# Optimization experiments

Measured on AMD Instinct MI355X. Metric: run time of the kernel, lower is better.

## Reference

```python
import jax, jax.numpy as jnp
import numpy as np

N_EMBD = 768
HEAD_SIZE = 64
B, T = 8, 4096


def setup_inputs() -> dict:
    key = jax.random.key(0)
    ks = jax.random.split(key, 7)
    s = 0.02  # small init scale for weights
    return {
        "x": jax.random.normal(ks[0], (B, T, N_EMBD), dtype=jnp.float32),
        "Wq": jax.random.normal(ks[1], (N_EMBD, HEAD_SIZE), dtype=jnp.float32) * s,
        "bq": jax.random.normal(ks[2], (HEAD_SIZE,), dtype=jnp.float32) * s,
        "Wk": jax.random.normal(ks[3], (N_EMBD, HEAD_SIZE), dtype=jnp.float32) * s,
        "bk": jax.random.normal(ks[4], (HEAD_SIZE,), dtype=jnp.float32) * s,
        "Wv": jax.random.normal(ks[5], (N_EMBD, HEAD_SIZE), dtype=jnp.float32) * s,
        "bv": jax.random.normal(ks[6], (HEAD_SIZE,), dtype=jnp.float32) * s,
    }


def reference(x, Wq, bq, Wk, bk, Wv, bv):
    # x: [B, T, C]; note: scale uses C = n_embd (input dim), per the original code.
    C = x.shape[-1]
    scale = jnp.asarray(C, x.dtype) ** -0.5
    q = x @ Wq + bq  # [B, T, H]
    k = x @ Wk + bk  # [B, T, H]
    v = x @ Wv + bv  # [B, T, H]
    wei = jnp.einsum("bqh,bkh->bqk", q, k) * scale  # [B, T, T]
    att = jax.nn.softmax(wei, axis=-1)
    # dropout p=0.0 (eval mode) -> identity
    out = jnp.einsum("bqk,bkh->bqh", att, v)  # [B, T, H]
    return out
```

## Files before the change

### kernel.cpp

```cpp
#include <hip/hip_runtime.h>
#include <stdint.h>

#define T_SEQ 4096
#define CEMB 768
#define HS 64

typedef __attribute__((ext_vector_type(8))) short bf16x8;
typedef __attribute__((ext_vector_type(16))) float f32x16;
typedef __attribute__((ext_vector_type(4))) unsigned int u32x4;

__device__ __forceinline__ short bfru(float f) {
    uint32_t u = __builtin_bit_cast(uint32_t, f);
    return (short)((u + 0x8000u) >> 16);
}
__device__ __forceinline__ uint32_t cvtpk_bf16(float lo, float hi) {
    uint32_t r;
    asm("v_cvt_pk_bf16_f32 %0, %1, %2" : "=v"(r) : "v"(lo), "v"(hi));
    return r;
}

#define QSCALE (0.036084391824351615f * 1.4426950408889634f)

__global__ __launch_bounds__(256) void prep_wt(const float* __restrict__ Wq,
                                               const float* __restrict__ Wk,
                                               const float* __restrict__ Wv,
                                               short* __restrict__ wtf) {
    const int p = blockIdx.x;
    const int tid = threadIdx.x;
    const int lane = tid & 63, jp = tid >> 6;
    const int l31 = lane & 31, lhi = lane >> 5;
    const int kq = p % 48, ct = p / 48;
    const int k = kq * 16 + lhi * 8 + jp * 2;
    const int nn = ct * 32 + l31;
    const float* W = nn < 64 ? Wq : (nn < 128 ? Wk : Wv);
    const int col = nn & 63;
    uint32_t lo = (uint16_t)bfru(W[k * 64 + col]);
    uint32_t hi = (uint16_t)bfru(W[(k + 1) * 64 + col]);
    *(uint32_t*)&wtf[(p * 64 + lane) * 8 + jp * 2] = lo | (hi << 16);
}

__global__ __launch_bounds__(256) void qkv_proj(const float* __restrict__ x,
        const float* __restrict__ bq, const float* __restrict__ bk, const float* __restrict__ bv,
        const short* __restrict__ wtf,
        short* __restrict__ qo, short* __restrict__ ko, short* __restrict__ vto) {
    __shared__ short S[64 * 72];

    const int tid  = threadIdx.x;
    const int wave = tid >> 6, lane = tid & 63;
    const int l31  = lane & 31, lhi = lane >> 5;
    const int rg   = wave & 1;
    const int ctb  = (wave >> 1) * 3;
    const int rowbase = blockIdx.x * 64;

    f32x16 acc[3];
    #pragma unroll
    for (int c = 0; c < 3; ++c) {
        const int ct = ctb + c, nn = ct * 32 + l31;
        const float bb = nn < 64 ? bq[nn] : (nn < 128 ? bk[nn - 64] : bv[nn - 128]);
        #pragma unroll
        for (int r = 0; r < 16; ++r) acc[c][r] = bb;
    }

    const int sr = tid >> 2, sseg = (tid & 3) * 16;
    for (int kt = 0; kt < 12; ++kt) {
        const float4* src = (const float4*)(x + (long)(rowbase + sr) * CEMB + kt * 64 + sseg);
        float4 f0 = src[0], f1 = src[1], f2 = src[2], f3 = src[3];
        bf16x8 w0, w1;
        w0[0]=bfru(f0.x); w0[1]=bfru(f0.y); w0[2]=bfru(f0.z); w0[3]=bfru(f0.w);
        w0[4]=bfru(f1.x); w0[5]=bfru(f1.y); w0[6]=bfru(f1.z); w0[7]=bfru(f1.w);
        w1[0]=bfru(f2.x); w1[1]=bfru(f2.y); w1[2]=bfru(f2.z); w1[3]=bfru(f2.w);
        w1[4]=bfru(f3.x); w1[5]=bfru(f3.y); w1[6]=bfru(f3.z); w1[7]=bfru(f3.w);
        *(bf16x8*)&S[sr * 72 + sseg]     = w0;
        *(bf16x8*)&S[sr * 72 + sseg + 8] = w1;
        __syncthreads();
        #pragma unroll
        for (int kc = 0; kc < 4; ++kc) {
            bf16x8 af = *(const bf16x8*)&S[(rg * 32 + l31) * 72 + kc * 16 + lhi * 8];
            #pragma unroll
            for (int c = 0; c < 3; ++c) {
                bf16x8 wf = *(const bf16x8*)&wtf[((ctb + c) * 48 + kt * 4 + kc) * 512 + lane * 8];
                acc[c] = __builtin_amdgcn_mfma_f32_32x32x16_bf16(af, wf, acc[c], 0, 0, 0);
            }
        }
        __syncthreads();
    }

    #pragma unroll
    for (int c = 0; c < 3; ++c) {
        const int ct = ctb + c;
        if (ct < 2) {
            #pragma unroll
            for (int r = 0; r < 16; ++r) {
                const int row = rg * 32 + (r & 3) + 8 * (r >> 2) + 4 * lhi;
                qo[(long)(rowbase + row) * HS + ct * 32 + l31] = bfru(acc[c][r] * QSCALE);
            }
        } else if (ct < 4) {
            #pragma unroll
            for (int r = 0; r < 16; ++r) {
                const int row = rg * 32 + (r & 3) + 8 * (r >> 2) + 4 * lhi;
                ko[(long)(rowbase + row) * HS + (ct - 2) * 32 + l31] = bfru(acc[c][r]);
            }
        } else {
            #pragma unroll
            for (int r = 0; r < 16; ++r) {
                const int row = rg * 32 + (r & 3) + 8 * (r >> 2) + 4 * lhi;
                S[((ct - 4) * 32 + l31) * 72 + row] = bfru(acc[c][r]);
            }
        }
    }
    __syncthreads();
    if (tid < 128) {
        const int vcol = tid >> 1, hh = tid & 1;
        const int b = rowbase >> 12, t0 = rowbase & 4095;
        short* dst = vto + ((long)b * HS + vcol) * T_SEQ + t0 + hh * 32;
        #pragma unroll
        for (int i = 0; i < 4; ++i)
            *(bf16x8*)(dst + i * 8) = *(const bf16x8*)&S[vcol * 72 + hh * 32 + i * 8];
    }
}

__global__ __launch_bounds__(256, 2) void attn(const short* __restrict__ qm,
        const short* __restrict__ km, const short* __restrict__ vtm,
        float* __restrict__ Op, float* __restrict__ lp, const int ks,
        float* __restrict__ outdirect) {
    __shared__ short Klds[2][64 * 72];
    __shared__ short Vlds[2][64 * 72];
    __shared__ float Lred[4][2][32];

    const int tid  = threadIdx.x;
    const int wave = tid >> 6, lane = tid & 63;
    const int l31  = lane & 31, lhi = lane >> 5;
    const int idx  = blockIdx.x;
    const int b = idx & 7, s = (idx >> 3) % ks, qt = idx / (8 * ks);
    const int slab = T_SEQ / ks, nkt = slab / 64;

    const short* qb = qm + ((long)b * T_SEQ + qt * 256 + wave * 64) * HS;
    const short* kb = km + ((long)b * T_SEQ + s * slab) * HS;
    const short* vb = vtm + (long)b * HS * T_SEQ + s * slab;

    bf16x8 qf[2][4];
    #pragma unroll
    for (int qs = 0; qs < 2; ++qs)
        #pragma unroll
        for (int kc = 0; kc < 4; ++kc)
            qf[qs][kc] = *(const bf16x8*)&qb[(qs * 32 + l31) * HS + kc * 16 + lhi * 8];

    f32x16 oacc[2][2] = {};
    float lsum[2] = {0.f, 0.f};

    const int sr = tid >> 2, sc = (tid & 3) * 16;
    const short* kp = kb + sr * HS + sc;
    const short* vp = vb + sr * T_SEQ + sc;

    bf16x8 kr0 = *(const bf16x8*)kp, kr1 = *(const bf16x8*)(kp + 8);
    bf16x8 vr0 = *(const bf16x8*)vp, vr1 = *(const bf16x8*)(vp + 8);
    *(bf16x8*)&Klds[0][sr * 72 + sc]     = kr0;
    *(bf16x8*)&Klds[0][sr * 72 + sc + 8] = kr1;
    *(bf16x8*)&Vlds[0][sr * 72 + sc]     = vr0;
    *(bf16x8*)&Vlds[0][sr * 72 + sc + 8] = vr1;
    __syncthreads();

    for (int kt = 0; kt < nkt; ++kt) {
        const int cur = kt & 1;
        const bool pfe = (kt + 1 < nkt);
        if (pfe) {
            const short* kp2 = kp + (kt + 1) * (64 * HS);
            const short* vp2 = vp + (kt + 1) * 64;
            kr0 = *(const bf16x8*)kp2; kr1 = *(const bf16x8*)(kp2 + 8);
            vr0 = *(const bf16x8*)vp2; vr1 = *(const bf16x8*)(vp2 + 8);
        }
        const short* Kc = Klds[cur];
        const short* Vc = Vlds[cur];
        #pragma unroll
        for (int ct = 0; ct < 2; ++ct) {
            const short* krow = &Kc[(ct * 32 + l31) * 72 + lhi * 8];
            bf16x8 kf0 = *(const bf16x8*)(krow);
            bf16x8 kf1 = *(const bf16x8*)(krow + 16);
            bf16x8 kf2 = *(const bf16x8*)(krow + 32);
            bf16x8 kf3 = *(const bf16x8*)(krow + 48);
            const short* vrow = &Vc[l31 * 72 + ct * 32 + lhi * 8];
            bf16x8 vf00 = *(const bf16x8*)(vrow);
            bf16x8 vf10 = *(const bf16x8*)(vrow + 16);
            bf16x8 vf01 = *(const bf16x8*)(vrow + 32 * 72);
            bf16x8 vf11 = *(const bf16x8*)(vrow + 32 * 72 + 16);
            #pragma unroll
            for (int qs = 0; qs < 2; ++qs) {
                f32x16 z = {};
                z = __builtin_amdgcn_mfma_f32_32x32x16_bf16(kf0, qf[qs][0], z, 0, 0, 0);
                z = __builtin_amdgcn_mfma_f32_32x32x16_bf16(kf1, qf[qs][1], z, 0, 0, 0);
                z = __builtin_amdgcn_mfma_f32_32x32x16_bf16(kf2, qf[qs][2], z, 0, 0, 0);
                z = __builtin_amdgcn_mfma_f32_32x32x16_bf16(kf3, qf[qs][3], z, 0, 0, 0);
                #pragma unroll
                for (int r = 0; r < 16; ++r) z[r] = __builtin_amdgcn_exp2f(z[r]);
                lsum[qs] += (((z[0]+z[1])+(z[2]+z[3])) + ((z[4]+z[5])+(z[6]+z[7])))
                          + (((z[8]+z[9])+(z[10]+z[11])) + ((z[12]+z[13])+(z[14]+z[15])));
                uint32_t x0 = cvtpk_bf16(z[0],  z[1]),  y0 = cvtpk_bf16(z[4],  z[5]);
                uint32_t x1 = cvtpk_bf16(z[2],  z[3]),  y1 = cvtpk_bf16(z[6],  z[7]);
                uint32_t x2 = cvtpk_bf16(z[8],  z[9]),  y2 = cvtpk_bf16(z[12], z[13]);
                uint32_t x3 = cvtpk_bf16(z[10], z[11]), y3 = cvtpk_bf16(z[14], z[15]);
                asm("v_permlane32_swap_b32 %0, %1" : "+v"(x0), "+v"(y0));
                asm("v_permlane32_swap_b32 %0, %1" : "+v"(x1), "+v"(y1));
                asm("v_permlane32_swap_b32 %0, %1" : "+v"(x2), "+v"(y2));
                asm("v_permlane32_swap_b32 %0, %1" : "+v"(x3), "+v"(y3));
                u32x4 t0 = {x0, x1, y0, y1};
                u32x4 t1 = {x2, x3, y2, y3};
                bf16x8 pa0 = __builtin_bit_cast(bf16x8, t0);
                bf16x8 pa1 = __builtin_bit_cast(bf16x8, t1);
                oacc[qs][0] = __builtin_amdgcn_mfma_f32_32x32x16_bf16(pa0, vf00, oacc[qs][0], 0, 0, 0);
                oacc[qs][1] = __builtin_amdgcn_mfma_f32_32x32x16_bf16(pa0, vf01, oacc[qs][1], 0, 0, 0);
                oacc[qs][0] = __builtin_amdgcn_mfma_f32_32x32x16_bf16(pa1, vf10, oacc[qs][0], 0, 0, 0);
                oacc[qs][1] = __builtin_amdgcn_mfma_f32_32x32x16_bf16(pa1, vf11, oacc[qs][1], 0, 0, 0);
            }
        }
        if (pfe) {
            const int nxt = cur ^ 1;
            *(bf16x8*)&Klds[nxt][sr * 72 + sc]     = kr0;
            *(bf16x8*)&Klds[nxt][sr * 72 + sc + 8] = kr1;
            *(bf16x8*)&Vlds[nxt][sr * 72 + sc]     = vr0;
            *(bf16x8*)&Vlds[nxt][sr * 72 + sc + 8] = vr1;
        }
        __syncthreads();
    }

    #pragma unroll
    for (int qs = 0; qs < 2; ++qs) lsum[qs] += __shfl_xor(lsum[qs], 32);

    const long rowg = (long)b * T_SEQ + qt * 256 + wave * 64;
    if (outdirect) {
        if (lhi == 0) { Lred[wave][0][l31] = lsum[0]; Lred[wave][1][l31] = lsum[1]; }
        __syncthreads();
        float* ob = outdirect + rowg * HS;
        #pragma unroll
        for (int qs = 0; qs < 2; ++qs)
            #pragma unroll
            for (int ht = 0; ht < 2; ++ht)
                #pragma unroll
                for (int r = 0; r < 16; ++r) {
                    const int row = (r & 3) + 8 * (r >> 2) + 4 * lhi;
                    ob[(long)(qs * 32 + row) * HS + ht * 32 + l31] =
                        oacc[qs][ht][r] / Lred[wave][qs][row];
                }
    } else {
        float* op = Op + ((long)s * 32768 + rowg) * HS;
        #pragma unroll
        for (int qs = 0; qs < 2; ++qs)
            #pragma unroll
            for (int ht = 0; ht < 2; ++ht)
                #pragma unroll
                for (int r = 0; r < 16; ++r) {
                    const int row = (r & 3) + 8 * (r >> 2) + 4 * lhi;
                    op[(qs * 32 + row) * HS + ht * 32 + l31] = oacc[qs][ht][r];
                }
        if (lhi == 0) {
            lp[(long)s * 32768 + rowg + l31]      = lsum[0];
            lp[(long)s * 32768 + rowg + 32 + l31] = lsum[1];
        }
    }
}

__global__ __launch_bounds__(256) void combine(const float4* __restrict__ Op,
        const float* __restrict__ lp, float4* __restrict__ out, const int ks) {
    const int idx = blockIdx.x * 256 + threadIdx.x;
    const int row = idx >> 4, h4 = idx & 15;
    float ox = 0.f, oy = 0.f, oz = 0.f, ow = 0.f, l = 0.f;
    for (int s = 0; s < ks; ++s) {
        float4 t = Op[(long)(s * 32768 + row) * 16 + h4];
        ox += t.x; oy += t.y; oz += t.z; ow += t.w;
        l += lp[s * 32768 + row];
    }
    const float inv = 1.0f / l;
    float4 o; o.x = ox * inv; o.y = oy * inv; o.z = oz * inv; o.w = ow * inv;
    out[(long)row * 16 + h4] = o;
}

extern "C" void kernel_launch(void* const* d_in, const int* in_sizes, int n_in,
                              void* d_out, int out_size, void* d_ws, size_t ws_size,
                              hipStream_t stream) {
    const float* x  = (const float*)d_in[0];
    const float* Wq = (const float*)d_in[1];
    const float* bq = (const float*)d_in[2];
    const float* Wk = (const float*)d_in[3];
    const float* bk = (const float*)d_in[4];
    const float* Wv = (const float*)d_in[5];
    const float* bv = (const float*)d_in[6];

    char* ws = (char*)d_ws;
    short* qo  = (short*)(ws);
    short* ko  = (short*)(ws + (4u << 20));
    short* vto = (short*)(ws + (8u << 20));
    short* wtf = (short*)(ws + (12u << 20));
    const size_t opOff = 12582912u + 294912u;
    float* Op = (float*)(ws + opOff);

    const size_t per_s = 8388608u + 131072u;
    int ks = (ws_size >= opOff + 4 * per_s) ? 4
           : (ws_size >= opOff + 2 * per_s) ? 2 : 1;
    float* lp = (float*)(ws + opOff + (size_t)ks * 8388608u);

    prep_wt<<<288, 256, 0, stream>>>(Wq, Wk, Wv, wtf);
    qkv_proj<<<512, 256, 0, stream>>>(x, bq, bk, bv, wtf, qo, ko, vto);
    attn<<<128 * ks, 256, 0, stream>>>(qo, ko, vto, Op, lp, ks,
                                       ks == 1 ? (float*)d_out : nullptr);
    if (ks > 1)
        combine<<<2048, 256, 0, stream>>>((const float4*)Op, lp, (float4*)d_out, ks);
}
```

Measured before the change: 217.4 us.

## Double-buffer x tiles in QKV projection and interleave QK MFMAs with setprio

The QKV projection kernel now double-buffers the LDS staging tile and prefetches the next x slice into registers while MFMAs run on the current one. This removes one barrier per k-step and hides global load latency. In the attention kernel, the two query sub-tiles' QK^T MFMA chains are interleaved so they can overlap, and s_setprio raises wave priority around MFMA bursts. The cost is twice the LDS in the projection kernel and more live registers in attention, which could hurt occupancy.

New measurement: 229.8 us. 1.06x slower.

```diff
diff --git a/kernel.cpp b/kernel.cpp
--- a/kernel.cpp
+++ b/kernel.cpp
@@ -43,7 +43,7 @@
         const float* __restrict__ bq, const float* __restrict__ bk, const float* __restrict__ bv,
         const short* __restrict__ wtf,
         short* __restrict__ qo, short* __restrict__ ko, short* __restrict__ vto) {
-    __shared__ short S[64 * 72];
+    __shared__ short S[2][64 * 72];
 
     const int tid  = threadIdx.x;
     const int wave = tid >> 6, lane = tid & 63;
@@ -62,25 +62,46 @@
     }
 
     const int sr = tid >> 2, sseg = (tid & 3) * 16;
-    for (int kt = 0; kt < 12; ++kt) {
-        const float4* src = (const float4*)(x + (long)(rowbase + sr) * CEMB + kt * 64 + sseg);
-        float4 f0 = src[0], f1 = src[1], f2 = src[2], f3 = src[3];
+    const float* xrow = x + (long)(rowbase + sr) * CEMB + sseg;
+    const short* wfb = wtf + (long)ctb * 48 * 512 + lane * 8;
+
+    float4 f0, f1, f2, f3;
+    {   const float4* src = (const float4*)xrow;
+        f0 = src[0]; f1 = src[1]; f2 = src[2]; f3 = src[3];
         bf16x8 w0, w1;
         w0[0]=bfru(f0.x); w0[1]=bfru(f0.y); w0[2]=bfru(f0.z); w0[3]=bfru(f0.w);
         w0[4]=bfru(f1.x); w0[5]=bfru(f1.y); w0[6]=bfru(f1.z); w0[7]=bfru(f1.w);
         w1[0]=bfru(f2.x); w1[1]=bfru(f2.y); w1[2]=bfru(f2.z); w1[3]=bfru(f2.w);
         w1[4]=bfru(f3.x); w1[5]=bfru(f3.y); w1[6]=bfru(f3.z); w1[7]=bfru(f3.w);
-        *(bf16x8*)&S[sr * 72 + sseg]     = w0;
-        *(bf16x8*)&S[sr * 72 + sseg + 8] = w1;
-        __syncthreads();
+        *(bf16x8*)&S[0][sr * 72 + sseg]     = w0;
+        *(bf16x8*)&S[0][sr * 72 + sseg + 8] = w1;
+    }
+    __syncthreads();
+
+    for (int kt = 0; kt < 12; ++kt) {
+        const int cur = kt & 1;
+        const bool pfe = (kt < 11);
+        if (pfe) {
+            const float4* src = (const float4*)(xrow + (kt + 1) * 64);
+            f0 = src[0]; f1 = src[1]; f2 = src[2]; f3 = src[3];
+        }
         #pragma unroll
         for (int kc = 0; kc < 4; ++kc) {
-            bf16x8 af = *(const bf16x8*)&S[(rg * 32 + l31) * 72 + kc * 16 + lhi * 8];
+            bf16x8 af = *(const bf16x8*)&S[cur][(rg * 32 + l31) * 72 + kc * 16 + lhi * 8];
             #pragma unroll
             for (int c = 0; c < 3; ++c) {
-                bf16x8 wf = *(const bf16x8*)&wtf[((ctb + c) * 48 + kt * 4 + kc) * 512 + lane * 8];
+                bf16x8 wf = *(const bf16x8*)(wfb + ((c * 48 + kt * 4 + kc) << 9));
                 acc[c] = __builtin_amdgcn_mfma_f32_32x32x16_bf16(af, wf, acc[c], 0, 0, 0);
             }
+        }
+        if (pfe) {
+            bf16x8 w0, w1;
+            w0[0]=bfru(f0.x); w0[1]=bfru(f0.y); w0[2]=bfru(f0.z); w0[3]=bfru(f0.w);
+            w0[4]=bfru(f1.x); w0[5]=bfru(f1.y); w0[6]=bfru(f1.z); w0[7]=bfru(f1.w);
+            w1[0]=bfru(f2.x); w1[1]=bfru(f2.y); w1[2]=bfru(f2.z); w1[3]=bfru(f2.w);
+            w1[4]=bfru(f3.x); w1[5]=bfru(f3.y); w1[6]=bfru(f3.z); w1[7]=bfru(f3.w);
+            *(bf16x8*)&S[cur ^ 1][sr * 72 + sseg]     = w0;
+            *(bf16x8*)&S[cur ^ 1][sr * 72 + sseg + 8] = w1;
         }
         __syncthreads();
     }
@@ -104,7 +125,7 @@
             #pragma unroll
             for (int r = 0; r < 16; ++r) {
                 const int row = rg * 32 + (r & 3) + 8 * (r >> 2) + 4 * lhi;
-                S[((ct - 4) * 32 + l31) * 72 + row] = bfru(acc[c][r]);
+                S[0][((ct - 4) * 32 + l31) * 72 + row] = bfru(acc[c][r]);
             }
         }
     }
@@ -115,7 +136,7 @@
         short* dst = vto + ((long)b * HS + vcol) * T_SEQ + t0 + hh * 32;
         #pragma unroll
         for (int i = 0; i < 4; ++i)
-            *(bf16x8*)(dst + i * 8) = *(const bf16x8*)&S[vcol * 72 + hh * 32 + i * 8];
+            *(bf16x8*)(dst + i * 8) = *(const bf16x8*)&S[0][vcol * 72 + hh * 32 + i * 8];
     }
 }
 
@@ -183,21 +204,28 @@
             bf16x8 vf10 = *(const bf16x8*)(vrow + 16);
             bf16x8 vf01 = *(const bf16x8*)(vrow + 32 * 72);
             bf16x8 vf11 = *(const bf16x8*)(vrow + 32 * 72 + 16);
-            #pragma unroll
-            for (int qs = 0; qs < 2; ++qs) {
-                f32x16 z = {};
-                z = __builtin_amdgcn_mfma_f32_32x32x16_bf16(kf0, qf[qs][0], z, 0, 0, 0);
-                z = __builtin_amdgcn_mfma_f32_32x32x16_bf16(kf1, qf[qs][1], z, 0, 0, 0);
-                z = __builtin_amdgcn_mfma_f32_32x32x16_bf16(kf2, qf[qs][2], z, 0, 0, 0);
-                z = __builtin_amdgcn_mfma_f32_32x32x16_bf16(kf3, qf[qs][3], z, 0, 0, 0);
-                #pragma unroll
-                for (int r = 0; r < 16; ++r) z[r] = __builtin_amdgcn_exp2f(z[r]);
-                lsum[qs] += (((z[0]+z[1])+(z[2]+z[3])) + ((z[4]+z[5])+(z[6]+z[7])))
-                          + (((z[8]+z[9])+(z[10]+z[11])) + ((z[12]+z[13])+(z[14]+z[15])));
-                uint32_t x0 = cvtpk_bf16(z[0],  z[1]),  y0 = cvtpk_bf16(z[4],  z[5]);
-                uint32_t x1 = cvtpk_bf16(z[2],  z[3]),  y1 = cvtpk_bf16(z[6],  z[7]);
-                uint32_t x2 = cvtpk_bf16(z[8],  z[9]),  y2 = cvtpk_bf16(z[12], z[13]);
-                uint32_t x3 = cvtpk_bf16(z[10], z[11]), y3 = cvtpk_bf16(z[14], z[15]);
+
+            f32x16 z0 = {}, z1 = {};
+            __builtin_amdgcn_s_setprio(1);
+            z0 = __builtin_amdgcn_mfma_f32_32x32x16_bf16(kf0, qf[0][0], z0, 0, 0, 0);
+            z1 = __builtin_amdgcn_mfma_f32_32x32x16_bf16(kf0, qf[1][0], z1, 0, 0, 0);
+            z0 = __builtin_amdgcn_mfma_f32_32x32x16_bf16(kf1, qf[0][1], z0, 0, 0, 0);
+            z1 = __builtin_amdgcn_mfma_f32_32x32x16_bf16(kf1, qf[1][1], z1, 0, 0, 0);
+            z0 = __builtin_amdgcn_mfma_f32_32x32x16_bf16(kf2, qf[0][2], z0, 0, 0, 0);
+            z1 = __builtin_amdgcn_mfma_f32_32x32x16_bf16(kf2, qf[1][2], z1, 0, 0, 0);
+            z0 = __builtin_amdgcn_mfma_f32_32x32x16_bf16(kf3, qf[0][3], z0, 0, 0, 0);
+            z1 = __builtin_amdgcn_mfma_f32_32x32x16_bf16(kf3, qf[1][3], z1, 0, 0, 0);
+            __builtin_amdgcn_s_setprio(0);
+
+            #pragma unroll
+            for (int r = 0; r < 16; ++r) z0[r] = __builtin_amdgcn_exp2f(z0[r]);
+            lsum[0] += (((z0[0]+z0[1])+(z0[2]+z0[3])) + ((z0[4]+z0[5])+(z0[6]+z0[7])))
+                     + (((z0[8]+z0[9])+(z0[10]+z0[11])) + ((z0[12]+z0[13])+(z0[14]+z0[15])));
+            {
+                uint32_t x0 = cvtpk_bf16(z0[0],  z0[1]),  y0 = cvtpk_bf16(z0[4],  z0[5]);
+                uint32_t x1 = cvtpk_bf16(z0[2],  z0[3]),  y1 = cvtpk_bf16(z0[6],  z0[7]);
+                uint32_t x2 = cvtpk_bf16(z0[8],  z0[9]),  y2 = cvtpk_bf16(z0[12], z0[13]);
+                uint32_t x3 = cvtpk_bf16(z0[10], z0[11]), y3 = cvtpk_bf16(z0[14], z0[15]);
                 asm("v_permlane32_swap_b32 %0, %1" : "+v"(x0), "+v"(y0));
                 asm("v_permlane32_swap_b32 %0, %1" : "+v"(x1), "+v"(y1));
                 asm("v_permlane32_swap_b32 %0, %1" : "+v"(x2), "+v"(y2));
@@ -206,10 +234,36 @@
                 u32x4 t1 = {x2, x3, y2, y3};
                 bf16x8 pa0 = __builtin_bit_cast(bf16x8, t0);
                 bf16x8 pa1 = __builtin_bit_cast(bf16x8, t1);
-                oacc[qs][0] = __builtin_amdgcn_mfma_f32_32x32x16_bf16(pa0, vf00, oacc[qs][0], 0, 0, 0);
-                oacc[qs][1] = __builtin_amdgcn_mfma_f32_32x32x16_bf16(pa0, vf01, oacc[qs][1], 0, 0, 0);
-                oacc[qs][0] = __builtin_amdgcn_mfma_f32_32x32x16_bf16(pa1, vf10, oacc[qs][0], 0, 0, 0);
-                oacc[qs][1] = __builtin_amdgcn_mfma_f32_32x32x16_bf16(pa1, vf11, oacc[qs][1], 0, 0, 0);
+                __builtin_amdgcn_s_setprio(1);
+                oacc[0][0] = __builtin_amdgcn_mfma_f32_32x32x16_bf16(pa0, vf00, oacc[0][0], 0, 0, 0);
+                oacc[0][1] = __builtin_amdgcn_mfma_f32_32x32x16_bf16(pa0, vf01, oacc[0][1], 0, 0, 0);
+                oacc[0][0] = __builtin_amdgcn_mfma_f32_32x32x16_bf16(pa1, vf10, oacc[0][0], 0, 0, 0);
+                oacc[0][1] = __builtin_amdgcn_mfma_f32_32x32x16_bf16(pa1, vf11, oacc[0][1], 0, 0, 0);
+                __builtin_amdgcn_s_setprio(0);
+            }
+            #pragma unroll
+            for (int r = 0; r < 16; ++r) z1[r] = __builtin_amdgcn_exp2f(z1[r]);
+            lsum[1] += (((z1[0]+z1[1])+(z1[2]+z1[3])) + ((z1[4]+z1[5])+(z1[6]+z1[7])))
+                     + (((z1[8]+z1[9])+(z1[10]+z1[11])) + ((z1[12]+z1[13])+(z1[14]+z1[15])));
+            {
+                uint32_t x0 = cvtpk_bf16(z1[0],  z1[1]),  y0 = cvtpk_bf16(z1[4],  z1[5]);
+                uint32_t x1 = cvtpk_bf16(z1[2],  z1[3]),  y1 = cvtpk_bf16(z1[6],  z1[7]);
+                uint32_t x2 = cvtpk_bf16(z1[8],  z1[9]),  y2 = cvtpk_bf16(z1[12], z1[13]);
+                uint32_t x3 = cvtpk_bf16(z1[10], z1[11]), y3 = cvtpk_bf16(z1[14], z1[15]);
+                asm("v_permlane32_swap_b32 %0, %1" : "+v"(x0), "+v"(y0));
+                asm("v_permlane32_swap_b32 %0, %1" : "+v"(x1), "+v"(y1));
+                asm("v_permlane32_swap_b32 %0, %1" : "+v"(x2), "+v"(y2));
+                asm("v_permlane32_swap_b32 %0, %1" : "+v"(x3), "+v"(y3));
+                u32x4 t0 = {x0, x1, y0, y1};
+                u32x4 t1 = {x2, x3, y2, y3};
+                bf16x8 pa0 = __builtin_bit_cast(bf16x8, t0);
+                bf16x8 pa1 = __builtin_bit_cast(bf16x8, t1);
+                __builtin_amdgcn_s_setprio(1);
+                oacc[1][0] = __builtin_amdgcn_mfma_f32_32x32x16_bf16(pa0, vf00, oacc[1][0], 0, 0, 0);
+                oacc[1][1] = __builtin_amdgcn_mfma_f32_32x32x16_bf16(pa0, vf01, oacc[1][1], 0, 0, 0);
+                oacc[1][0] = __builtin_amdgcn_mfma_f32_32x32x16_bf16(pa1, vf10, oacc[1][0], 0, 0, 0);
+                oacc[1][1] = __builtin_amdgcn_mfma_f32_32x32x16_bf16(pa1, vf11, oacc[1][1], 0, 0, 0);
+                __builtin_amdgcn_s_setprio(0);
             }
         }
         if (pfe) {
```

## Double-buffer and register-prefetch x tiles in QKV projection kernel

Applied to the files above, without the earlier changes.

The QKV projection loop now keeps two LDS buffers and prefetches x tiles two iterations ahead into registers. Each tile is converted to bf16 and stored into the alternate buffer while MFMAs run on the current one, which drops one barrier per iteration. Weight fragments for the whole k-tile are also loaded up front into registers. This hides global load latency behind compute at the cost of more registers (launch bounds now ask for 2 blocks) and double the LDS.

Measured after the change: 216.2 us. No clear change (-0.5%).

```diff
diff --git a/kernel.cpp b/kernel.cpp
--- a/kernel.cpp
+++ b/kernel.cpp
@@ -39,11 +39,11 @@
     *(uint32_t*)&wtf[(p * 64 + lane) * 8 + jp * 2] = lo | (hi << 16);
 }
 
-__global__ __launch_bounds__(256) void qkv_proj(const float* __restrict__ x,
+__global__ __launch_bounds__(256, 2) void qkv_proj(const float* __restrict__ x,
         const float* __restrict__ bq, const float* __restrict__ bk, const float* __restrict__ bv,
         const short* __restrict__ wtf,
         short* __restrict__ qo, short* __restrict__ ko, short* __restrict__ vto) {
-    __shared__ short S[64 * 72];
+    __shared__ short S[2][64 * 72];
 
     const int tid  = threadIdx.x;
     const int wave = tid >> 6, lane = tid & 63;
@@ -62,25 +62,62 @@
     }
 
     const int sr = tid >> 2, sseg = (tid & 3) * 16;
+    const float* xrow = x + (long)(rowbase + sr) * CEMB + sseg;
+    const short* wfb = wtf + (long)ctb * 48 * 512 + lane * 8;
+
+    float4 RA0, RA1, RA2, RA3;
+    float4 RB0, RB1, RB2, RB3;
+    {
+        const float4* s0 = (const float4*)xrow;
+        RA0 = s0[0]; RA1 = s0[1]; RA2 = s0[2]; RA3 = s0[3];
+        const float4* s1 = (const float4*)(xrow + 64);
+        RB0 = s1[0]; RB1 = s1[1]; RB2 = s1[2]; RB3 = s1[3];
+        bf16x8 w0, w1;
+        w0[0]=bfru(RA0.x); w0[1]=bfru(RA0.y); w0[2]=bfru(RA0.z); w0[3]=bfru(RA0.w);
+        w0[4]=bfru(RA1.x); w0[5]=bfru(RA1.y); w0[6]=bfru(RA1.z); w0[7]=bfru(RA1.w);
+        w1[0]=bfru(RA2.x); w1[1]=bfru(RA2.y); w1[2]=bfru(RA2.z); w1[3]=bfru(RA2.w);
+        w1[4]=bfru(RA3.x); w1[5]=bfru(RA3.y); w1[6]=bfru(RA3.z); w1[7]=bfru(RA3.w);
+        *(bf16x8*)&S[0][sr * 72 + sseg]     = w0;
+        *(bf16x8*)&S[0][sr * 72 + sseg + 8] = w1;
+    }
+    __syncthreads();
+
+    #pragma unroll
     for (int kt = 0; kt < 12; ++kt) {
-        const float4* src = (const float4*)(x + (long)(rowbase + sr) * CEMB + kt * 64 + sseg);
-        float4 f0 = src[0], f1 = src[1], f2 = src[2], f3 = src[3];
-        bf16x8 w0, w1;
-        w0[0]=bfru(f0.x); w0[1]=bfru(f0.y); w0[2]=bfru(f0.z); w0[3]=bfru(f0.w);
-        w0[4]=bfru(f1.x); w0[5]=bfru(f1.y); w0[6]=bfru(f1.z); w0[7]=bfru(f1.w);
-        w1[0]=bfru(f2.x); w1[1]=bfru(f2.y); w1[2]=bfru(f2.z); w1[3]=bfru(f2.w);
-        w1[4]=bfru(f3.x); w1[5]=bfru(f3.y); w1[6]=bfru(f3.z); w1[7]=bfru(f3.w);
-        *(bf16x8*)&S[sr * 72 + sseg]     = w0;
-        *(bf16x8*)&S[sr * 72 + sseg + 8] = w1;
-        __syncthreads();
+        const int cur = kt & 1;
+        bf16x8 wfr[12];
+        #pragma unroll
+        for (int kc = 0; kc < 4; ++kc)
+            #pragma unroll
+            for (int c = 0; c < 3; ++c)
+                wfr[kc * 3 + c] = *(const bf16x8*)(wfb + ((c * 48 + kt * 4 + kc) << 9));
+        if (kt + 2 < 12) {
+            const float4* sn = (const float4*)(xrow + (kt + 2) * 64);
+            if (cur == 0) { RA0 = sn[0]; RA1 = sn[1]; RA2 = sn[2]; RA3 = sn[3]; }
+            else          { RB0 = sn[0]; RB1 = sn[1]; RB2 = sn[2]; RB3 = sn[3]; }
+        }
         #pragma unroll
         for (int kc = 0; kc < 4; ++kc) {
-            bf16x8 af = *(const bf16x8*)&S[(rg * 32 + l31) * 72 + kc * 16 + lhi * 8];
-            #pragma unroll
-            for (int c = 0; c < 3; ++c) {
-                bf16x8 wf = *(const bf16x8*)&wtf[((ctb + c) * 48 + kt * 4 + kc) * 512 + lane * 8];
-                acc[c] = __builtin_amdgcn_mfma_f32_32x32x16_bf16(af, wf, acc[c], 0, 0, 0);
-            }
+            bf16x8 af = *(const bf16x8*)&S[cur][(rg * 32 + l31) * 72 + kc * 16 + lhi * 8];
+            acc[0] = __builtin_amdgcn_mfma_f32_32x32x16_bf16(af, wfr[kc * 3 + 0], acc[0], 0, 0, 0);
+            acc[1] = __builtin_amdgcn_mfma_f32_32x32x16_bf16(af, wfr[kc * 3 + 1], acc[1], 0, 0, 0);
+            acc[2] = __builtin_amdgcn_mfma_f32_32x32x16_bf16(af, wfr[kc * 3 + 2], acc[2], 0, 0, 0);
+        }
+        if (kt + 1 < 12) {
+            bf16x8 w0, w1;
+            if (cur == 0) {
+                w0[0]=bfru(RB0.x); w0[1]=bfru(RB0.y); w0[2]=bfru(RB0.z); w0[3]=bfru(RB0.w);
+                w0[4]=bfru(RB1.x); w0[5]=bfru(RB1.y); w0[6]=bfru(RB1.z); w0[7]=bfru(RB1.w);
+                w1[0]=bfru(RB2.x); w1[1]=bfru(RB2.y); w1[2]=bfru(RB2.z); w1[3]=bfru(RB2.w);
+                w1[4]=bfru(RB3.x); w1[5]=bfru(RB3.y); w1[6]=bfru(RB3.z); w1[7]=bfru(RB3.w);
+            } else {
+                w0[0]=bfru(RA0.x); w0[1]=bfru(RA0.y); w0[2]=bfru(RA0.z); w0[3]=bfru(RA0.w);
+                w0[4]=bfru(RA1.x); w0[5]=bfru(RA1.y); w0[6]=bfru(RA1.z); w0[7]=bfru(RA1.w);
+                w1[0]=bfru(RA2.x); w1[1]=bfru(RA2.y); w1[2]=bfru(RA2.z); w1[3]=bfru(RA2.w);
+                w1[4]=bfru(RA3.x); w1[5]=bfru(RA3.y); w1[6]=bfru(RA3.z); w1[7]=bfru(RA3.w);
+            }
+            *(bf16x8*)&S[cur ^ 1][sr * 72 + sseg]     = w0;
+            *(bf16x8*)&S[cur ^ 1][sr * 72 + sseg + 8] = w1;
         }
         __syncthreads();
     }
@@ -104,7 +141,7 @@
             #pragma unroll
             for (int r = 0; r < 16; ++r) {
                 const int row = rg * 32 + (r & 3) + 8 * (r >> 2) + 4 * lhi;
-                S[((ct - 4) * 32 + l31) * 72 + row] = bfru(acc[c][r]);
+                S[0][((ct - 4) * 32 + l31) * 72 + row] = bfru(acc[c][r]);
             }
         }
     }
@@ -115,7 +152,7 @@
         short* dst = vto + ((long)b * HS + vcol) * T_SEQ + t0 + hh * 32;
         #pragma unroll
         for (int i = 0; i < 4; ++i)
-            *(bf16x8*)(dst + i * 8) = *(const bf16x8*)&S[vcol * 72 + hh * 32 + i * 8];
+            *(bf16x8*)(dst + i * 8) = *(const bf16x8*)&S[0][vcol * 72 + hh * 32 + i * 8];
     }
 }
 
```

## Restructure QKV projection into 32-row tiles with double-buffered x prefetch

Applied to the files above, without the earlier changes.

The QKV projection kernel now processes 32 rows per block instead of 64, launching twice as many blocks with a 4-blocks-per-CU launch bound. Each wave owns one Q/K column tile plus optionally one V tile. The x tile is double-buffered in shared memory with register prefetch two steps ahead, which removes one barrier per k-step and overlaps global loads with MFMA work. The V transpose store is also redone for the smaller tile. The trade-off is uneven work across waves, since only two of four waves compute V, and the weight fragments are loaded by twice as many blocks.

Result: no change. 213.8 us (-1.6%).

```diff
diff --git a/kernel.cpp b/kernel.cpp
--- a/kernel.cpp
+++ b/kernel.cpp
@@ -39,83 +39,113 @@
     *(uint32_t*)&wtf[(p * 64 + lane) * 8 + jp * 2] = lo | (hi << 16);
 }
 
-__global__ __launch_bounds__(256) void qkv_proj(const float* __restrict__ x,
+__global__ __launch_bounds__(256, 4) void qkv_proj(const float* __restrict__ x,
         const float* __restrict__ bq, const float* __restrict__ bk, const float* __restrict__ bv,
         const short* __restrict__ wtf,
         short* __restrict__ qo, short* __restrict__ ko, short* __restrict__ vto) {
-    __shared__ short S[64 * 72];
+    __shared__ short S[2][32 * 72];
 
     const int tid  = threadIdx.x;
     const int wave = tid >> 6, lane = tid & 63;
     const int l31  = lane & 31, lhi = lane >> 5;
-    const int rg   = wave & 1;
-    const int ctb  = (wave >> 1) * 3;
-    const int rowbase = blockIdx.x * 64;
-
-    f32x16 acc[3];
+    const int rowbase = blockIdx.x * 32;
+    const int ctA  = wave;
+    const bool hasB = (wave < 2);
+    const int ctB  = wave + 4;
+
+    f32x16 acc0, acc1;
+    {
+        const int nnA = ctA * 32 + l31;
+        const float bA = nnA < 64 ? bq[nnA] : bk[nnA - 64];
+        float bB = 0.f;
+        if (hasB) bB = bv[(ctB - 4) * 32 + l31];
+        #pragma unroll
+        for (int r = 0; r < 16; ++r) { acc0[r] = bA; acc1[r] = bB; }
+    }
+
+    const int sr = tid >> 3, sseg = (tid & 7) * 8;
+    const float* xrow = x + (long)(rowbase + sr) * CEMB + sseg;
+    const short* wfA = wtf + (long)ctA * 48 * 512 + lane * 8;
+    const short* wfB = wtf + (long)ctB * 48 * 512 + lane * 8;
+
+    float4 RA0, RA1, RB0, RB1;
+    {
+        const float4* s0 = (const float4*)xrow;
+        RA0 = s0[0]; RA1 = s0[1];
+        const float4* s1 = (const float4*)(xrow + 64);
+        RB0 = s1[0]; RB1 = s1[1];
+        bf16x8 w;
+        w[0]=bfru(RA0.x); w[1]=bfru(RA0.y); w[2]=bfru(RA0.z); w[3]=bfru(RA0.w);
+        w[4]=bfru(RA1.x); w[5]=bfru(RA1.y); w[6]=bfru(RA1.z); w[7]=bfru(RA1.w);
+        *(bf16x8*)&S[0][sr * 72 + sseg] = w;
+    }
+    __syncthreads();
+
     #pragma unroll
-    for (int c = 0; c < 3; ++c) {
-        const int ct = ctb + c, nn = ct * 32 + l31;
-        const float bb = nn < 64 ? bq[nn] : (nn < 128 ? bk[nn - 64] : bv[nn - 128]);
-        #pragma unroll
-        for (int r = 0; r < 16; ++r) acc[c][r] = bb;
-    }
-
-    const int sr = tid >> 2, sseg = (tid & 3) * 16;
     for (int kt = 0; kt < 12; ++kt) {
-        const float4* src = (const float4*)(x + (long)(rowbase + sr) * CEMB + kt * 64 + sseg);
-        float4 f0 = src[0], f1 = src[1], f2 = src[2], f3 = src[3];
-        bf16x8 w0, w1;
-        w0[0]=bfru(f0.x); w0[1]=bfru(f0.y); w0[2]=bfru(f0.z); w0[3]=bfru(f0.w);
-        w0[4]=bfru(f1.x); w0[5]=bfru(f1.y); w0[6]=bfru(f1.z); w0[7]=bfru(f1.w);
-        w1[0]=bfru(f2.x); w1[1]=bfru(f2.y); w1[2]=bfru(f2.z); w1[3]=bfru(f2.w);
-        w1[4]=bfru(f3.x); w1[5]=bfru(f3.y); w1[6]=bfru(f3.z); w1[7]=bfru(f3.w);
-        *(bf16x8*)&S[sr * 72 + sseg]     = w0;
-        *(bf16x8*)&S[sr * 72 + sseg + 8] = w1;
+        const int cur = kt & 1;
+        bf16x8 wA[4], wB[4];
+        #pragma unroll
+        for (int kc = 0; kc < 4; ++kc)
+            wA[kc] = *(const bf16x8*)(wfA + ((kt * 4 + kc) << 9));
+        if (hasB) {
+            #pragma unroll
+            for (int kc = 0; kc < 4; ++kc)
+                wB[kc] = *(const bf16x8*)(wfB + ((kt * 4 + kc) << 9));
+        }
+        if (kt + 2 < 12) {
+            const float4* sn = (const float4*)(xrow + (kt + 2) * 64);
+            if (cur == 0) { RA0 = sn[0]; RA1 = sn[1]; }
+            else          { RB0 = sn[0]; RB1 = sn[1]; }
+        }
+        #pragma unroll
+        for (int kc = 0; kc < 4; ++kc) {
+            bf16x8 af = *(const bf16x8*)&S[cur][l31 * 72 + kc * 16 + lhi * 8];
+            acc0 = __builtin_amdgcn_mfma_f32_32x32x16_bf16(af, wA[kc], acc0, 0, 0, 0);
+            if (hasB)
+                acc1 = __builtin_amdgcn_mfma_f32_32x32x16_bf16(af, wB[kc], acc1, 0, 0, 0);
+        }
+        if (kt + 1 < 12) {
+            bf16x8 w;
+            if (cur == 0) {
+                w[0]=bfru(RB0.x); w[1]=bfru(RB0.y); w[2]=bfru(RB0.z); w[3]=bfru(RB0.w);
+                w[4]=bfru(RB1.x); w[5]=bfru(RB1.y); w[6]=bfru(RB1.z); w[7]=bfru(RB1.w);
+            } else {
+                w[0]=bfru(RA0.x); w[1]=bfru(RA0.y); w[2]=bfru(RA0.z); w[3]=bfru(RA0.w);
+                w[4]=bfru(RA1.x); w[5]=bfru(RA1.y); w[6]=bfru(RA1.z); w[7]=bfru(RA1.w);
+            }
+            *(bf16x8*)&S[cur ^ 1][sr * 72 + sseg] = w;
+        }
         __syncthreads();
-        #pragma unroll
-        for (int kc = 0; kc < 4; ++kc) {
-            bf16x8 af = *(const bf16x8*)&S[(rg * 32 + l31) * 72 + kc * 16 + lhi * 8];
-            #pragma unroll
-            for (int c = 0; c < 3; ++c) {
-                bf16x8 wf = *(const bf16x8*)&wtf[((ctb + c) * 48 + kt * 4 + kc) * 512 + lane * 8];
-                acc[c] = __builtin_amdgcn_mfma_f32_32x32x16_bf16(af, wf, acc[c], 0, 0, 0);
-            }
-        }
-        __syncthreads();
-    }
-
-    #pragma unroll
-    for (int c = 0; c < 3; ++c) {
-        const int ct = ctb + c;
-        if (ct < 2) {
-            #pragma unroll
-            for (int r = 0; r < 16; ++r) {
-                const int row = rg * 32 + (r & 3) + 8 * (r >> 2) + 4 * lhi;
-                qo[(long)(rowbase + row) * HS + ct * 32 + l31] = bfru(acc[c][r] * QSCALE);
-            }
-        } else if (ct < 4) {
-            #pragma unroll
-            for (int r = 0; r < 16; ++r) {
-                const int row = rg * 32 + (r & 3) + 8 * (r >> 2) + 4 * lhi;
-                ko[(long)(rowbase + row) * HS + (ct - 2) * 32 + l31] = bfru(acc[c][r]);
-            }
-        } else {
-            #pragma unroll
-            for (int r = 0; r < 16; ++r) {
-                const int row = rg * 32 + (r & 3) + 8 * (r >> 2) + 4 * lhi;
-                S[((ct - 4) * 32 + l31) * 72 + row] = bfru(acc[c][r]);
-            }
+    }
+
+    if (ctA < 2) {
+        #pragma unroll
+        for (int r = 0; r < 16; ++r) {
+            const int row = (r & 3) + 8 * (r >> 2) + 4 * lhi;
+            qo[(long)(rowbase + row) * HS + ctA * 32 + l31] = bfru(acc0[r] * QSCALE);
+        }
+    } else {
+        #pragma unroll
+        for (int r = 0; r < 16; ++r) {
+            const int row = (r & 3) + 8 * (r >> 2) + 4 * lhi;
+            ko[(long)(rowbase + row) * HS + (ctA - 2) * 32 + l31] = bfru(acc0[r]);
+        }
+    }
+    short* Sf = (short*)S;
+    if (hasB) {
+        #pragma unroll
+        for (int r = 0; r < 16; ++r) {
+            const int row = (r & 3) + 8 * (r >> 2) + 4 * lhi;
+            Sf[((ctB - 4) * 32 + l31) * 40 + row] = bfru(acc1[r]);
         }
     }
     __syncthreads();
-    if (tid < 128) {
-        const int vcol = tid >> 1, hh = tid & 1;
+    {
+        const int vcol = tid >> 2, tseg = (tid & 3) * 8;
         const int b = rowbase >> 12, t0 = rowbase & 4095;
-        short* dst = vto + ((long)b * HS + vcol) * T_SEQ + t0 + hh * 32;
-        #pragma unroll
-        for (int i = 0; i < 4; ++i)
-            *(bf16x8*)(dst + i * 8) = *(const bf16x8*)&S[vcol * 72 + hh * 32 + i * 8];
+        *(bf16x8*)(vto + ((long)b * HS + vcol) * T_SEQ + t0 + tseg)
+            = *(const bf16x8*)&Sf[vcol * 40 + tseg];
     }
 }
 
@@ -213,11 +243,12 @@
             }
         }
         if (pfe) {
-            const int nxt = cur ^ 1;
-            *(bf16x8*)&Klds[nxt][sr * 72 + sc]     = kr0;
-            *(bf16x8*)&Klds[nxt][sr * 72 + sc + 8] = kr1;
-            *(bf16x8*)&Vlds[nxt][sr * 72 + sc]     = vr0;
-            *(bf16x8*)&Vlds[nxt][sr * 72 + sc + 8] = vr1;
+            short* Kn = (short*)Klds[cur ^ 1];
+            short* Vn = (short*)Vlds[cur ^ 1];
+            *(bf16x8*)&Kn[sr * 72 + sc]     = kr0;
+            *(bf16x8*)&Kn[sr * 72 + sc + 8] = kr1;
+            *(bf16x8*)&Vn[sr * 72 + sc]     = vr0;
+            *(bf16x8*)&Vn[sr * 72 + sc + 8] = vr1;
         }
         __syncthreads();
     }
@@ -298,7 +329,7 @@
     float* lp = (float*)(ws + opOff + (size_t)ks * 8388608u);
 
     prep_wt<<<288, 256, 0, stream>>>(Wq, Wk, Wv, wtf);
-    qkv_proj<<<512, 256, 0, stream>>>(x, bq, bk, bv, wtf, qo, ko, vto);
+    qkv_proj<<<1024, 256, 0, stream>>>(x, bq, bk, bv, wtf, qo, ko, vto);
     attn<<<128 * ks, 256, 0, stream>>>(qo, ko, vto, Op, lp, ks,
                                        ks == 1 ? (float*)d_out : nullptr);
     if (ks > 1)
```
